# Kernel optimization log

Measured on AMD Instinct MI355X. Metric: run time of the kernel, lower is better.

Reference implementation:

```python
import jax, jax.numpy as jnp
import numpy as np

DIM = 1024

def setup_inputs() -> dict:
    key = jax.random.key(0)
    ks = jax.random.split(key, 7)
    s = 1.0 / np.sqrt(DIM)  # roughly match nn.Linear init scale
    return {
        "x": jax.random.normal(ks[0], (4, 2048, DIM), dtype=jnp.float32),
        "Wq": jax.random.normal(ks[1], (DIM, DIM), dtype=jnp.float32) * s,
        "bq": jax.random.normal(ks[2], (DIM,), dtype=jnp.float32) * s,
        "Wk": jax.random.normal(ks[3], (DIM, DIM), dtype=jnp.float32) * s,
        "bk": jax.random.normal(ks[4], (DIM,), dtype=jnp.float32) * s,
        "Wv": jax.random.normal(ks[5], (DIM, DIM), dtype=jnp.float32) * s,
        "bv": jax.random.normal(ks[6], (DIM,), dtype=jnp.float32) * s,
    }

def reference(x, Wq, bq, Wk, bk, Wv, bv):
    # torch Linear: y = x @ W.T + b
    C = x.shape[-1]
    scale = C ** (-0.5)
    q = jnp.einsum('bnc,dc->bnd', x, Wq) + bq
    k = jnp.einsum('bnc,dc->bnd', x, Wk) + bk
    v = jnp.einsum('bnc,dc->bnd', x, Wv) + bv
    attn = jnp.einsum('bnd,bmd->bnm', q, k) * scale  # [B,N,N]
    attn = jax.nn.softmax(attn, axis=-1)
    out = jnp.einsum('bnm,bmd->bnd', attn, v)
    return out
```

## Files before the change

### kernel.cpp

```cpp
#include <hip/hip_runtime.h>

#define SEQ  2048
#define DIM  1024
#define NTOK 8192
#define NQKV 3072

typedef __attribute__((ext_vector_type(8))) __bf16 bf16x8;
typedef __attribute__((ext_vector_type(4))) float  f32x4;

__device__ __forceinline__ unsigned short f2bf(float f) {
    unsigned int u = __float_as_uint(f);
    u += 0x7fffu + ((u >> 16) & 1u);
    return (unsigned short)(u >> 16);
}

__device__ __forceinline__ float bfu2f(unsigned int lo16) {
    return __uint_as_float(lo16 << 16);
}

__device__ __forceinline__ void load_lds_128(const unsigned short* g, unsigned short* l) {
    __builtin_amdgcn_global_load_lds(
        (const __attribute__((address_space(1))) void*)g,
        (__attribute__((address_space(3))) void*)l, 16, 0, 0);
}

#define BAR()    asm volatile("s_barrier" ::: "memory")
#define WAITL0() do { asm volatile("s_waitcnt lgkmcnt(0)" ::: "memory"); \
                      __builtin_amdgcn_sched_barrier(0); } while (0)

template <int MODE>
__global__ __launch_bounds__(512, 2)
void gemm256(const unsigned short* __restrict__ A, const unsigned short* __restrict__ B,
             void* __restrict__ Cv,
             const float* __restrict__ b0, const float* __restrict__ b1,
             const float* __restrict__ b2, unsigned short* __restrict__ vt,
             const float* __restrict__ inv_rs,
             int K, int lda, int ldb, int ldc,
             long sA, long sB, long sC, float alpha)
{
    constexpr int AT = 256 * 64;
    constexpr int BT = 128 * 64;
    __shared__ __align__(16) unsigned short As[3 * AT];
    __shared__ __align__(16) unsigned short Bs[3 * BT];

    const int tid  = threadIdx.x;
    const int wave = tid >> 6;
    const int lane = tid & 63;
    const int l4   = lane & 15;
    const int lh   = lane >> 4;
    const int wm   = wave >> 1;
    const int wn   = wave & 1;

    const int m0 = blockIdx.x * 256;
    const int n0 = blockIdx.y * 128;
    const int z  = blockIdx.z;
    A += (long)z * sA;
    B += (long)z * sB;

    const int r0 = tid >> 3;
    const int gc = (tid & 7) ^ (r0 & 7);
    const unsigned short* Ag = A + (long)(m0 + r0) * lda + gc * 8;
    const unsigned short* Bg = B + (long)(n0 + r0) * ldb + gc * 8;
    unsigned short* Al = As + tid * 8;
    unsigned short* Bl = Bs + tid * 8;

    const int NT = K >> 6;

    auto stage = [&](int t, int slot, int ph) {
        const long kof = (long)t * 64;
        unsigned short* al = Al + slot * AT;
        unsigned short* bl = Bl + slot * BT;
        if (ph == 0) {
            load_lds_128(Ag + kof,                          al);
            load_lds_128(Ag + kof + (long)64 * lda,         al + 4096);
            load_lds_128(Bg + kof,                          bl);
        } else {
            load_lds_128(Ag + kof + (long)128 * lda,        al + 8192);
            load_lds_128(Ag + kof + (long)192 * lda,        al + 12288);
            load_lds_128(Bg + kof + (long)64 * ldb,         bl + 4096);
        }
    };

    const int aoff = (wm * 64 + l4) * 64;
    const int boff = (wn * 64 + l4) * 64;
    const int cs0  = ((0 + lh) ^ (lane & 7)) * 8;
    const int cs1  = ((4 + lh) ^ (lane & 7)) * 8;

    f32x4 acc[4][4] = {};

    stage(0, 0, 0); stage(0, 0, 1);
    stage(1, 1, 0); stage(1, 1, 1);
    asm volatile("s_waitcnt vmcnt(6)" ::: "memory");
    BAR();

    int sl = 0;
    for (int t = 0; t < NT; ++t) {
        const unsigned short* Ab = As + sl * AT + aoff;
        const unsigned short* Bb = Bs + sl * BT + boff;
        const int st = (sl >= 1) ? sl - 1 : 2;
        const bool pf = (t + 2 < NT);
        bf16x8 a[4], b[4];

#pragma unroll
        for (int mf = 0; mf < 4; ++mf) a[mf] = *(const bf16x8*)(Ab + mf * 1024 + cs0);
#pragma unroll
        for (int nf = 0; nf < 4; ++nf) b[nf] = *(const bf16x8*)(Bb + nf * 1024 + cs0);
        if (pf) stage(t + 2, st, 0);
        BAR();
        WAITL0();
        __builtin_amdgcn_s_setprio(1);
#pragma unroll
        for (int mf = 0; mf < 4; ++mf)
#pragma unroll
            for (int nf = 0; nf < 4; ++nf)
                acc[mf][nf] = __builtin_amdgcn_mfma_f32_16x16x32_bf16(
                    a[mf], b[nf], acc[mf][nf], 0, 0, 0);
        __builtin_amdgcn_s_setprio(0);

#pragma unroll
        for (int mf = 0; mf < 4; ++mf) a[mf] = *(const bf16x8*)(Ab + mf * 1024 + cs1);
#pragma unroll
        for (int nf = 0; nf < 4; ++nf) b[nf] = *(const bf16x8*)(Bb + nf * 1024 + cs1);
        if (pf) stage(t + 2, st, 1);
        BAR();
        WAITL0();
        __builtin_amdgcn_s_setprio(1);
#pragma unroll
        for (int mf = 0; mf < 4; ++mf)
#pragma unroll
            for (int nf = 0; nf < 4; ++nf)
                acc[mf][nf] = __builtin_amdgcn_mfma_f32_16x16x32_bf16(
                    a[mf], b[nf], acc[mf][nf], 0, 0, 0);
        __builtin_amdgcn_s_setprio(0);

        if (t < NT - 2) asm volatile("s_waitcnt vmcnt(6)" ::: "memory");
        else            asm volatile("s_waitcnt vmcnt(0)" ::: "memory");
        BAR();
        sl = (sl == 2) ? 0 : sl + 1;
    }

    const int r0c = m0 + wm * 64 + lh * 4;
    const int c0c = n0 + wn * 64 + l4;

    if (MODE == 0) {
        if (n0 >= 2048) {
#pragma unroll
            for (int nf = 0; nf < 4; ++nf) {
                const int d = c0c + nf * 16 - 2048;
                const float bias = b2[d];
#pragma unroll
                for (int mf = 0; mf < 4; ++mf) {
                    const int row = r0c + mf * 16;
                    const int bb = row >> 11;
                    const int mm = row & 2047;
                    ushort4 u;
                    u.x = f2bf(acc[mf][nf][0] + bias);
                    u.y = f2bf(acc[mf][nf][1] + bias);
                    u.z = f2bf(acc[mf][nf][2] + bias);
                    u.w = f2bf(acc[mf][nf][3] + bias);
                    *(ushort4*)(vt + ((long)bb * DIM + d) * SEQ + mm) = u;
                }
            }
        } else {
            unsigned short* C16 = (unsigned short*)Cv;
#pragma unroll
            for (int nf = 0; nf < 4; ++nf) {
                const int col = c0c + nf * 16;
                const float bias = (col >= 1024) ? b1[col - 1024] : b0[col];
#pragma unroll
                for (int mf = 0; mf < 4; ++mf)
#pragma unroll
                    for (int r = 0; r < 4; ++r)
                        C16[(long)(r0c + mf * 16 + r) * ldc + col] =
                            f2bf(acc[mf][nf][r] + bias);
            }
        }
    } else if (MODE == 1) {
        float* C = (float*)Cv + (long)z * sC;
        const float* ir = inv_rs + (long)z * SEQ;
#pragma unroll
        for (int mf = 0; mf < 4; ++mf) {
            const int row = r0c + mf * 16;
            const float4 inv4 = *(const float4*)(ir + row);
#pragma unroll
            for (int nf = 0; nf < 4; ++nf) {
                const int col = c0c + nf * 16;
                C[(long)(row + 0) * ldc + col] = acc[mf][nf][0] * inv4.x;
                C[(long)(row + 1) * ldc + col] = acc[mf][nf][1] * inv4.y;
                C[(long)(row + 2) * ldc + col] = acc[mf][nf][2] * inv4.z;
                C[(long)(row + 3) * ldc + col] = acc[mf][nf][3] * inv4.w;
            }
        }
    } else {
        unsigned short* C16 = (unsigned short*)Cv + (long)z * sC;
#pragma unroll
        for (int nf = 0; nf < 4; ++nf) {
            const int col = c0c + nf * 16;
#pragma unroll
            for (int mf = 0; mf < 4; ++mf)
#pragma unroll
                for (int r = 0; r < 4; ++r)
                    C16[(long)(r0c + mf * 16 + r) * ldc + col] =
                        f2bf(__expf(acc[mf][nf][r] * alpha));
        }
    }
}

__global__ __launch_bounds__(256)
void cvt_x(const float* __restrict__ src, unsigned short* __restrict__ dst, int n4)
{
    int i = blockIdx.x * 256 + threadIdx.x;
    if (i < n4) {
        float4 f = ((const float4*)src)[i];
        ushort4 u;
        u.x = f2bf(f.x); u.y = f2bf(f.y); u.z = f2bf(f.z); u.w = f2bf(f.w);
        ((ushort4*)dst)[i] = u;
    }
}

__global__ __launch_bounds__(256)
void cvt_w3(const float* __restrict__ Wq, const float* __restrict__ Wk,
            const float* __restrict__ Wv, unsigned short* __restrict__ dst)
{
    const int sel = blockIdx.y;
    const float* src = (sel == 0) ? Wq : ((sel == 1) ? Wk : Wv);
    const int i = blockIdx.x * 256 + threadIdx.x;
    float4 f = ((const float4*)src)[i];
    ushort4 u;
    u.x = f2bf(f.x); u.y = f2bf(f.y); u.z = f2bf(f.z); u.w = f2bf(f.w);
    ((ushort4*)(dst + (long)sel * DIM * DIM))[i] = u;
}

__global__ __launch_bounds__(256)
void rowsum_inv(const unsigned short* __restrict__ P, float* __restrict__ inv_rs)
{
    const int row  = blockIdx.x * 4 + (threadIdx.x >> 6);
    const int lane = threadIdx.x & 63;
    const unsigned short* pr = P + (long)row * SEQ;

    float s = 0.f;
#pragma unroll
    for (int it = 0; it < 4; ++it) {
        uint4 u = *(const uint4*)(pr + (it * 64 + lane) * 8);
        s += bfu2f(u.x & 0xffffu) + __uint_as_float(u.x & 0xffff0000u);
        s += bfu2f(u.y & 0xffffu) + __uint_as_float(u.y & 0xffff0000u);
        s += bfu2f(u.z & 0xffffu) + __uint_as_float(u.z & 0xffff0000u);
        s += bfu2f(u.w & 0xffffu) + __uint_as_float(u.w & 0xffff0000u);
    }
    for (int off = 32; off > 0; off >>= 1)
        s += __shfl_xor(s, off);
    if (lane == 0) inv_rs[row] = 1.0f / s;
}

extern "C" void kernel_launch(void* const* d_in, const int* in_sizes, int n_in,
                              void* d_out, int out_size, void* d_ws, size_t ws_size,
                              hipStream_t stream)
{
    const float* x  = (const float*)d_in[0];
    const float* Wq = (const float*)d_in[1];
    const float* bq = (const float*)d_in[2];
    const float* Wk = (const float*)d_in[3];
    const float* bk = (const float*)d_in[4];
    const float* Wv = (const float*)d_in[5];
    const float* bv = (const float*)d_in[6];
    float* out = (float*)d_out;

    char* ws = (char*)d_ws;
    unsigned short* xb   = (unsigned short*)ws;
    unsigned short* Wb   = (unsigned short*)(ws + 16u * 1024 * 1024);
    unsigned short* qkv  = (unsigned short*)(ws + 64u * 1024 * 1024);
    unsigned short* vt   = (unsigned short*)(ws + 112u * 1024 * 1024);
    unsigned short* P    = (unsigned short*)(ws + 128u * 1024 * 1024);
    float*          irs  = (float*)(ws + 160u * 1024 * 1024);

    const float scale = 0.03125f;
    dim3 blk(256);
    dim3 blk512(512);

    cvt_x<<<NTOK * DIM / 4 / 256, blk, 0, stream>>>(x, xb, NTOK * DIM / 4);
    cvt_w3<<<dim3(DIM * DIM / 4 / 256, 3), blk, 0, stream>>>(Wq, Wk, Wv, Wb);

    gemm256<0><<<dim3(NTOK / 256, NQKV / 128), blk512, 0, stream>>>(
        xb, Wb, qkv, bq, bk, bv, vt, nullptr,
        DIM, DIM, DIM, NQKV, 0, 0, 0, 1.0f);

    gemm256<2><<<dim3(SEQ / 256, SEQ / 128, 4), blk512, 0, stream>>>(
        qkv, qkv + 1024, P, nullptr, nullptr, nullptr, nullptr, nullptr,
        DIM, NQKV, NQKV, SEQ,
        (long)SEQ * NQKV, (long)SEQ * NQKV, (long)SEQ * SEQ, scale);

    rowsum_inv<<<NTOK / 4, blk, 0, stream>>>(P, irs);

    gemm256<1><<<dim3(SEQ / 256, DIM / 128, 4), blk512, 0, stream>>>(
        P, vt, out, nullptr, nullptr, nullptr, nullptr, irs,
        SEQ, SEQ, SEQ, DIM,
        (long)SEQ * SEQ, (long)DIM * SEQ, (long)SEQ * DIM, 1.0f);
}
```

Baseline: 255.9 us.

## Double-buffer LDS fragment registers to overlap reads with MFMA

```diff
diff --git a/kernel.cpp b/kernel.cpp
--- a/kernel.cpp
+++ b/kernel.cpp
@@ -24,16 +24,14 @@
         (__attribute__((address_space(3))) void*)l, 16, 0, 0);
 }
 
-#define BAR()    asm volatile("s_barrier" ::: "memory")
-#define WAITL0() do { asm volatile("s_waitcnt lgkmcnt(0)" ::: "memory"); \
-                      __builtin_amdgcn_sched_barrier(0); } while (0)
+#define BAR() asm volatile("s_barrier" ::: "memory")
 
 template <int MODE>
 __global__ __launch_bounds__(512, 2)
 void gemm256(const unsigned short* __restrict__ A, const unsigned short* __restrict__ B,
              void* __restrict__ Cv,
-             const float* __restrict__ b0, const float* __restrict__ b1,
-             const float* __restrict__ b2, unsigned short* __restrict__ vt,
+             const float* __restrict__ b0v, const float* __restrict__ b1v,
+             const float* __restrict__ b2v, unsigned short* __restrict__ vt,
              const float* __restrict__ inv_rs,
              int K, int lda, int ldb, int ldc,
              long sA, long sB, long sC, float alpha)
@@ -87,56 +85,52 @@
     const int cs1  = ((4 + lh) ^ (lane & 7)) * 8;
 
     f32x4 acc[4][4] = {};
+    bf16x8 a0[4], b0[4], a1[4], b1[4];
+
+    auto ldfrag = [&](bf16x8 (&a)[4], bf16x8 (&b)[4],
+                      const unsigned short* Ab, const unsigned short* Bb, int cs) {
+#pragma unroll
+        for (int mf = 0; mf < 4; ++mf) a[mf] = *(const bf16x8*)(Ab + mf * 1024 + cs);
+#pragma unroll
+        for (int nf = 0; nf < 4; ++nf) b[nf] = *(const bf16x8*)(Bb + nf * 1024 + cs);
+    };
+    auto mfma16 = [&](bf16x8 (&a)[4], bf16x8 (&b)[4]) {
+        __builtin_amdgcn_s_setprio(1);
+#pragma unroll
+        for (int mf = 0; mf < 4; ++mf)
+#pragma unroll
+            for (int nf = 0; nf < 4; ++nf)
+                acc[mf][nf] = __builtin_amdgcn_mfma_f32_16x16x32_bf16(
+                    a[mf], b[nf], acc[mf][nf], 0, 0, 0);
+        __builtin_amdgcn_s_setprio(0);
+    };
 
     stage(0, 0, 0); stage(0, 0, 1);
     stage(1, 1, 0); stage(1, 1, 1);
     asm volatile("s_waitcnt vmcnt(6)" ::: "memory");
     BAR();
+    ldfrag(a0, b0, As + aoff, Bs + boff, cs0);
 
     int sl = 0;
     for (int t = 0; t < NT; ++t) {
         const unsigned short* Ab = As + sl * AT + aoff;
         const unsigned short* Bb = Bs + sl * BT + boff;
-        const int st = (sl >= 1) ? sl - 1 : 2;
-        const bool pf = (t + 2 < NT);
-        bf16x8 a[4], b[4];
-
-#pragma unroll
-        for (int mf = 0; mf < 4; ++mf) a[mf] = *(const bf16x8*)(Ab + mf * 1024 + cs0);
-#pragma unroll
-        for (int nf = 0; nf < 4; ++nf) b[nf] = *(const bf16x8*)(Bb + nf * 1024 + cs0);
-        if (pf) stage(t + 2, st, 0);
-        BAR();
-        WAITL0();
-        __builtin_amdgcn_s_setprio(1);
-#pragma unroll
-        for (int mf = 0; mf < 4; ++mf)
-#pragma unroll
-            for (int nf = 0; nf < 4; ++nf)
-                acc[mf][nf] = __builtin_amdgcn_mfma_f32_16x16x32_bf16(
-                    a[mf], b[nf], acc[mf][nf], 0, 0, 0);
-        __builtin_amdgcn_s_setprio(0);
-
-#pragma unroll
-        for (int mf = 0; mf < 4; ++mf) a[mf] = *(const bf16x8*)(Ab + mf * 1024 + cs1);
-#pragma unroll
-        for (int nf = 0; nf < 4; ++nf) b[nf] = *(const bf16x8*)(Bb + nf * 1024 + cs1);
-        if (pf) stage(t + 2, st, 1);
-        BAR();
-        WAITL0();
-        __builtin_amdgcn_s_setprio(1);
-#pragma unroll
-        for (int mf = 0; mf < 4; ++mf)
-#pragma unroll
-            for (int nf = 0; nf < 4; ++nf)
-                acc[mf][nf] = __builtin_amdgcn_mfma_f32_16x16x32_bf16(
-                    a[mf], b[nf], acc[mf][nf], 0, 0, 0);
-        __builtin_amdgcn_s_setprio(0);
-
+        const int st  = (sl >= 1) ? sl - 1 : 2;
+        const int nsl = (sl == 2) ? 0 : sl + 1;
+
+        ldfrag(a1, b1, Ab, Bb, cs1);
+        if (t + 2 < NT) stage(t + 2, st, 0);
+        mfma16(a0, b0);
+
+        if (t + 2 < NT) stage(t + 2, st, 1);
+        asm volatile("s_waitcnt lgkmcnt(0)" ::: "memory");
         if (t < NT - 2) asm volatile("s_waitcnt vmcnt(6)" ::: "memory");
         else            asm volatile("s_waitcnt vmcnt(0)" ::: "memory");
         BAR();
-        sl = (sl == 2) ? 0 : sl + 1;
+        if (t + 1 < NT)
+            ldfrag(a0, b0, As + nsl * AT + aoff, Bs + nsl * BT + boff, cs0);
+        mfma16(a1, b1);
+        sl = nsl;
     }
 
     const int r0c = m0 + wm * 64 + lh * 4;
@@ -147,7 +141,7 @@
 #pragma unroll
             for (int nf = 0; nf < 4; ++nf) {
                 const int d = c0c + nf * 16 - 2048;
-                const float bias = b2[d];
+                const float bias = b2v[d];
 #pragma unroll
                 for (int mf = 0; mf < 4; ++mf) {
                     const int row = r0c + mf * 16;
@@ -166,7 +160,7 @@
 #pragma unroll
             for (int nf = 0; nf < 4; ++nf) {
                 const int col = c0c + nf * 16;
-                const float bias = (col >= 1024) ? b1[col - 1024] : b0[col];
+                const float bias = (col >= 1024) ? b1v[col - 1024] : b0v[col];
 #pragma unroll
                 for (int mf = 0; mf < 4; ++mf)
 #pragma unroll
```

Result: faster. 244.0 us (-4.7%).
